# Performance work log

Hardware: AMD Instinct MI355X
Metric: run time of the kernel (lower is better)

Reference implementation:

```python
import jax, jax.numpy as jnp
import numpy as np

B, T, C, H = 4, 1024, 512, 4
D = C // H
N_LAYER, LAYER_ID = 12, 1


def setup_inputs() -> dict:
    key = jax.random.key(0)
    ks = jax.random.split(key, 10)
    w = lambda k, shape: 0.02 * jax.random.normal(k, shape, dtype=jnp.float32)

    r01 = LAYER_ID / (N_LAYER - 1)          # ratio_0_to_1
    r1a0 = 1.0 - LAYER_ID / N_LAYER          # ratio_1_to_almost0
    i = np.arange(C, dtype=np.float32)
    time_decay = (-5.0 + 8.0 * (i / (C - 1)) ** (0.7 + 1.3 * r01)).astype(np.float32)
    xv = i / C
    tm_q = (xv ** r1a0).astype(np.float32)[None, None, :]
    tm_k = (xv ** r1a0).astype(np.float32)[None, None, :]
    tm_v = ((xv ** r1a0) + 0.3 * r01).astype(np.float32)[None, None, :]
    tm_g = (xv ** (0.5 * r1a0)).astype(np.float32)[None, None, :]

    return dict(
        x=jax.random.normal(ks[0], (B, T, C), dtype=jnp.float32),
        ln1_g=jnp.ones((C,), jnp.float32), ln1_b=jnp.zeros((C,), jnp.float32),
        ln2_g=jnp.ones((C,), jnp.float32), ln2_b=jnp.zeros((C,), jnp.float32),
        time_decay=jnp.asarray(time_decay),
        tm_q=jnp.asarray(tm_q), tm_k=jnp.asarray(tm_k),
        tm_v=jnp.asarray(tm_v), tm_g=jnp.asarray(tm_g),
        Wq=w(ks[1], (C, C)), Wk=w(ks[2], (C, C)), Wv=w(ks[3], (C, C)),
        Wg=w(ks[4], (C, C)), Wo=w(ks[5], (C, C)),
        rms_scale=jnp.ones((C,), jnp.float32),
        W1=w(ks[6], (4 * C, C)), W2=w(ks[7], (C, 4 * C)),
    )


def layernorm(x, g, b, eps=1e-5):
    m = x.mean(-1, keepdims=True)
    v = ((x - m) ** 2).mean(-1, keepdims=True)
    return g * (x - m) / jnp.sqrt(v + eps) + b


def rmsnorm(x, scale, eps=1e-8):
    # matches: norm = ||x||_2 / sqrt(dim); out = scale * x / (norm + eps)
    norm = jnp.sqrt(jnp.sum(x * x, axis=-1, keepdims=True)) / (x.shape[-1] ** 0.5)
    return scale * (x / (norm + eps))


def lnssm_scan(q, k, v, lam):
    """Decayed linear-attention scan. q,k,v: [B,T,H,D]; lam: [H,D] (decay over k index).
    Returns S: [B,T,H,D] = q_t^T A_t, Zs: [B,T,H] = q_t . z_t."""
    qT, kT, vT = (jnp.moveaxis(a, 1, 0) for a in (q, k, v))  # [T,B,H,D]
    Bq = q.shape[0]
    A0 = jnp.zeros((Bq, q.shape[2], q.shape[3], q.shape[3]), q.dtype)
    z0 = jnp.zeros((Bq, q.shape[2], q.shape[3]), q.dtype)

    def step(carry, inp):
        A, z = carry
        qt, kt, vt = inp
        A = lam[None, :, :, None] * A + kt[..., None] * vt[..., None, :]  # [B,H,Dk,Dv]
        z = lam[None] * z + kt                                            # [B,H,Dk]
        St = jnp.einsum('bhi,bhij->bhj', qt, A)
        Zt = jnp.einsum('bhi,bhi->bh', qt, z)
        return (A, z), (St, Zt)

    _, (S, Zs) = jax.lax.scan(step, (A0, z0), (qT, kT, vT))
    return jnp.moveaxis(S, 0, 1), jnp.moveaxis(Zs, 0, 1)


def reference(x, ln1_g, ln1_b, ln2_g, ln2_b, time_decay, tm_q, tm_k, tm_v, tm_g,
              Wq, Wk, Wv, Wg, Wo, rms_scale, W1, W2):
    Bx, Tx, Cx = x.shape
    Hh, Dd = H, Cx // H

    # --- TimeMix on ln1(x) ---
    h = layernorm(x, ln1_g, ln1_b)
    xx = jnp.concatenate([jnp.zeros_like(h[:, :1]), h[:, :-1]], axis=1)  # time shift
    xq = h * tm_q + xx * (1 - tm_q)
    xk = h * tm_k + xx * (1 - tm_k)
    xv_ = h * tm_v + xx * (1 - tm_v)
    xg = h * tm_g + xx * (1 - tm_g)
    q = xq @ Wq.T
    k = xk @ Wk.T
    v = xv_ @ Wv.T
    g = jax.nn.sigmoid(xg @ Wg.T)
    q = jnp.exp(rmsnorm(q, rms_scale))
    k = jnp.exp(rmsnorm(k, rms_scale))

    lam = jnp.exp(-jnp.exp(time_decay)).reshape(Hh, Dd)
    qh = q.reshape(Bx, Tx, Hh, Dd)
    kh = k.reshape(Bx, Tx, Hh, Dd)
    vh = v.reshape(Bx, Tx, Hh, Dd)
    S, Zs = lnssm_scan(qh, kh, vh, lam)
    att = (S / Zs[..., None]).reshape(Bx, Tx, Cx)
    att = (g * att) @ Wo.T
    x = x + att

    # --- ChannelMix on ln2(x) ---
    h2 = layernorm(x, ln2_g, ln2_b)
    x = x + jax.nn.gelu(h2 @ W1.T, approximate=False) @ W2.T
    return x
```

## Files before the change

### kernel.cpp

```cpp
#include <hip/hip_runtime.h>
#include <math.h>

#define Bb 4
#define Tt 1024
#define Cc 512
#define Hh 4
#define Dd 128
#define Mrows (Bb*Tt)
#define NC 32
#define CL 32
#define AUGB_CB 18432

typedef unsigned short u16;
typedef __attribute__((ext_vector_type(8))) short bf16x8;
typedef __attribute__((ext_vector_type(4))) float f32x4;

__device__ __forceinline__ u16 f2bf(float f) {
  unsigned u = __float_as_uint(f);
  unsigned r = (u + 0x7fffu + ((u >> 16) & 1u)) >> 16;
  return (u16)r;
}
__device__ __forceinline__ float bf2f(u16 v) {
  return __uint_as_float((unsigned)v << 16);
}
__device__ __forceinline__ unsigned pack2(float a, float b) {
  return (unsigned)f2bf(a) | ((unsigned)f2bf(b) << 16);
}
__device__ __forceinline__ void unpack8(uint4 a, u16* o) {
  o[0]=(u16)a.x; o[1]=(u16)(a.x>>16);
  o[2]=(u16)a.y; o[3]=(u16)(a.y>>16);
  o[4]=(u16)a.z; o[5]=(u16)(a.z>>16);
  o[6]=(u16)a.w; o[7]=(u16)(a.w>>16);
}
__device__ __forceinline__ float rms_r(const float* __restrict__ ssqp, int zsel, int row) {
  const float* p = ssqp + (size_t)zsel*8*Mrows + row;
  float s2 = 0.f;
  #pragma unroll
  for (int u = 0; u < 8; ++u) s2 += p[(size_t)u*Mrows];
  float norm = sqrtf(s2) * 0.044194173824159216f;
  return 1.f / (norm + 1e-8f);
}

__global__ __launch_bounds__(256) void prep_kernel(const float* __restrict__ x,
    const float* __restrict__ g, const float* __restrict__ bta,
    const float* __restrict__ tmq, const float* __restrict__ tmk,
    const float* __restrict__ tmv, const float* __restrict__ tmg,
    u16* __restrict__ xqb, u16* __restrict__ xkb,
    u16* __restrict__ xvb, u16* __restrict__ xgb,
    const float* __restrict__ Wq, const float* __restrict__ Wk,
    const float* __restrict__ Wv, const float* __restrict__ Wg,
    const float* __restrict__ Wo, const float* __restrict__ W1,
    const float* __restrict__ W2, u16* __restrict__ wout)
{
  int tid = threadIdx.x;
  if (blockIdx.x >= 4096) {
    int blk = blockIdx.x - 4096;
    const float* src; u16* dst; int K, nshift;
    if (blk < 640) {
      int wsel = blk >> 7;
      src = wsel==0?Wq:wsel==1?Wk:wsel==2?Wv:wsel==3?Wg:Wo;
      dst = wout + (size_t)wsel*262144; K = 512; nshift = 9; blk &= 127;
    } else if (blk < 1152) {
      src = W1; dst = wout + (size_t)5*262144; K = 512; nshift = 11; blk -= 640;
    } else {
      src = W2; dst = wout + (size_t)5*262144 + 1048576; K = 2048; nshift = 9; blk -= 1152;
    }
    int i = blk*256 + tid;
    int n = i & ((1 << nshift) - 1), kg = i >> nshift;
    const float* p = src + (size_t)n * K + kg * 8;
    float4 a = *(const float4*)p, b = *(const float4*)(p + 4);
    uint4 o;
    o.x = pack2(a.x, a.y); o.y = pack2(a.z, a.w);
    o.z = pack2(b.x, b.y); o.w = pack2(b.z, b.w);
    *(uint4*)(dst + (size_t)i * 8) = o;
    return;
  }
  int m = blockIdx.x;
  const float* xr = x + (size_t)m * Cc;
  float v0 = xr[tid], v1 = xr[tid + 256];
  bool has = (m & (Tt-1)) != 0;
  float u0 = 0.f, u1 = 0.f;
  if (has) { u0 = xr[tid - Cc]; u1 = xr[(int)tid + 256 - Cc]; }
  float sa = v0 + v1, qa = v0*v0 + v1*v1;
  float sb = u0 + u1, qb2 = u0*u0 + u1*u1;
  #pragma unroll
  for (int off = 32; off > 0; off >>= 1) {
    sa += __shfl_down(sa, off, 64); qa += __shfl_down(qa, off, 64);
    sb += __shfl_down(sb, off, 64); qb2 += __shfl_down(qb2, off, 64);
  }
  __shared__ float r4[4][4];
  int w = tid >> 6;
  if ((tid & 63) == 0) { r4[w][0]=sa; r4[w][1]=qa; r4[w][2]=sb; r4[w][3]=qb2; }
  __syncthreads();
  float Sa = r4[0][0]+r4[1][0]+r4[2][0]+r4[3][0];
  float Qa = r4[0][1]+r4[1][1]+r4[2][1]+r4[3][1];
  float Sb = r4[0][2]+r4[1][2]+r4[2][2]+r4[3][2];
  float Qb = r4[0][3]+r4[1][3]+r4[2][3]+r4[3][3];
  float ma = Sa*(1.f/Cc), va = Qa*(1.f/Cc) - ma*ma, ia = rsqrtf(va + 1e-5f);
  float mb = Sb*(1.f/Cc), vb2 = Qb*(1.f/Cc) - mb*mb, ib = rsqrtf(vb2 + 1e-5f);
  #pragma unroll
  for (int half = 0; half < 2; ++half) {
    int c = tid + half*256;
    float v = half ? v1 : v0, u = half ? u1 : u0;
    float hv = g[c]*(v - ma)*ia + bta[c];
    float pv = has ? (g[c]*(u - mb)*ib + bta[c]) : 0.f;
    size_t off = ((size_t)(c >> 3) * Mrows + m) * 8 + (c & 7);
    float tq = tmq[c], tk = tmk[c], tv = tmv[c], tg = tmg[c];
    xqb[off] = f2bf(hv*tq + pv*(1.f-tq));
    xkb[off] = f2bf(hv*tk + pv*(1.f-tk));
    xvb[off] = f2bf(hv*tv + pv*(1.f-tv));
    xgb[off] = f2bf(hv*tg + pv*(1.f-tg));
  }
}

__global__ __launch_bounds__(256) void ln2b_kernel(const float* __restrict__ x,
    const float* __restrict__ p0,
    const float* __restrict__ g, const float* __restrict__ bta,
    float* __restrict__ x1, u16* __restrict__ out)
{
  int row = blockIdx.x, tid = threadIdx.x;
  size_t r0 = (size_t)row * Cc + tid, r1 = r0 + 256;
  float v0 = x[r0] + p0[r0];
  float v1 = x[r1] + p0[r1];
  x1[r0] = v0; x1[r1] = v1;
  float s = v0 + v1, s2 = v0*v0 + v1*v1;
  #pragma unroll
  for (int off = 32; off > 0; off >>= 1) {
    s  += __shfl_down(s,  off, 64);
    s2 += __shfl_down(s2, off, 64);
  }
  __shared__ float rs[4], rq[4];
  int w = tid >> 6;
  if ((tid & 63) == 0) { rs[w] = s; rq[w] = s2; }
  __syncthreads();
  float S  = rs[0]+rs[1]+rs[2]+rs[3];
  float S2 = rq[0]+rq[1]+rq[2]+rq[3];
  float mean = S * (1.0f/Cc);
  float var  = S2 * (1.0f/Cc) - mean*mean;
  float inv = rsqrtf(var + 1e-5f);
  int c0 = tid, c1 = tid + 256;
  float o0 = g[c0] * (v0-mean)*inv + bta[c0];
  float o1 = g[c1] * (v1-mean)*inv + bta[c1];
  out[((size_t)(c0 >> 3) * Mrows + row) * 8 + (c0 & 7)] = f2bf(o0);
  out[((size_t)(c1 >> 3) * Mrows + row) * 8 + (c1 & 7)] = f2bf(o1);
}

template<int MR, int NR, int KR>
__device__ __forceinline__ void gemm_core64(const u16* __restrict__ A,
    const u16* __restrict__ W, const float* __restrict__ res,
    float* __restrict__ outf, u16* __restrict__ outb, int act,
    int m0, int n0, u16* Asm, u16* Bsm, float* __restrict__ ssq)
{
  const int tid = threadIdx.x, w = tid >> 6, l = tid & 63;
  const int wr = w >> 1, wc = w & 1;
  f32x4 acc[2][2];
  #pragma unroll
  for (int i = 0; i < 2; ++i)
    #pragma unroll
    for (int j = 0; j < 2; ++j) acc[i][j] = (f32x4){0.f,0.f,0.f,0.f};
  const int kgl = l >> 4, rl = l & 15;
  const int q = w * 2;

  #define STAGE(KT, BUF) do {                                               \
    _Pragma("unroll")                                                       \
    for (int ii = 0; ii < 2; ++ii) {                                        \
      int qq = q + ii;                                                      \
      int isB = qq >> 2, kg = qq & 3;                                       \
      const u16* src = isB                                                  \
        ? W + ((size_t)((KT)*4 + kg) * NR + n0 + l) * 8                     \
        : A + ((size_t)((KT)*4 + kg) * MR + m0 + l) * 8;                    \
      u16* dst = (isB ? Bsm : Asm) + (BUF)*2048 + kg * 64 * 8;              \
      __builtin_amdgcn_global_load_lds(                                     \
          (const __attribute__((address_space(1))) void*)src,               \
          (__attribute__((address_space(3))) void*)dst, 16, 0, 0);          \
    }                                                                       \
  } while (0)

  constexpr int nk = KR >> 5;
  STAGE(0, 0); STAGE(1, 1);
  int cur = 0;
  for (int kt = 0; kt < nk; ++kt) {
    if (kt == nk - 1) asm volatile("s_waitcnt vmcnt(0)" ::: "memory");
    else              asm volatile("s_waitcnt vmcnt(2)" ::: "memory");
    __builtin_amdgcn_s_barrier();
    bf16x8 af[2], bfr[2];
    #pragma unroll
    for (int f = 0; f < 2; ++f)
      af[f] = *(const bf16x8*)&Asm[cur*2048 + (kgl*64 + wr*32 + f*16 + rl) * 8];
    #pragma unroll
    for (int f = 0; f < 2; ++f)
      bfr[f] = *(const bf16x8*)&Bsm[cur*2048 + (kgl*64 + wc*32 + f*16 + rl) * 8];
    if (kt + 2 < nk) {
      int nb = cur + 2; if (nb >= 3) nb -= 3;
      STAGE(kt + 2, nb);
    }
    __builtin_amdgcn_s_setprio(1);
    #pragma unroll
    for (int i = 0; i < 2; ++i)
      #pragma unroll
      for (int j = 0; j < 2; ++j)
        acc[i][j] = __builtin_amdgcn_mfma_f32_16x16x32_bf16(af[i], bfr[j], acc[i][j], 0, 0, 0);
    __builtin_amdgcn_s_setprio(0);
    if (++cur == 3) cur = 0;
  }
  #undef STAGE

  const int rbase = (l >> 4) * 4, cn = l & 15;
  #pragma unroll
  for (int i = 0; i < 2; ++i) {
    #pragma unroll
    for (int j = 0; j < 2; ++j) {
      #pragma unroll
      for (int r = 0; r < 4; ++r) {
        int m = m0 + wr*32 + i*16 + rbase + r;
        int n = n0 + wc*32 + j*16 + cn;
        float vv = acc[i][j][r];
        if (res) vv += res[(size_t)m * NR + n];
        if (act == 1) vv = 0.5f*vv*(1.f + erff(vv * 0.70710678118f));
        else if (act == 2) vv = 1.f/(1.f + expf(-vv));
        if (outb) outb[((size_t)(n >> 3) * MR + m) * 8 + (n & 7)] = f2bf(vv);
        else outf[(size_t)m * NR + n] = vv;
      }
    }
  }

  if (ssq) {
    __syncthreads();
    float* red2 = (float*)Asm;
    #pragma unroll
    for (int i = 0; i < 2; ++i) {
      #pragma unroll
      for (int r = 0; r < 4; ++r) {
        int row_local = wr*32 + i*16 + rbase + r;
        float sq = 0.f;
        #pragma unroll
        for (int j = 0; j < 2; ++j) { float t = acc[i][j][r]; sq += t*t; }
        red2[row_local*32 + wc*16 + cn] = sq;
      }
    }
    __syncthreads();
    if (tid < 64) {
      float ssum = 0.f;
      #pragma unroll
      for (int u2 = 0; u2 < 32; ++u2) ssum += red2[tid*32 + u2];
      ssq[m0 + tid] = ssum;
    }
  }
}

__global__ __launch_bounds__(256) void gemm_qkvg(const u16* __restrict__ xall,
    const u16* __restrict__ Wall, u16* __restrict__ outall, float* __restrict__ ssqp)
{
  __shared__ __align__(16) u16 Asm[3*2048];
  __shared__ __align__(16) u16 Bsm[3*2048];
  int z = blockIdx.z;
  const size_t E = (size_t)Mrows * Cc;
  float* ssq = (z < 2) ? ssqp + ((size_t)z*8 + blockIdx.x)*Mrows : nullptr;
  gemm_core64<Mrows,512,512>(xall + z*E, Wall + (size_t)z*262144, nullptr,
            nullptr, outall + z*E, z == 3 ? 2 : 0,
            blockIdx.y * 64, blockIdx.x * 64, Asm, Bsm, ssq);
}

__global__ __launch_bounds__(256) void gemm_wo(const u16* __restrict__ A,
    const u16* __restrict__ W, float* __restrict__ outf)
{
  __shared__ __align__(16) u16 Asm[3*2048];
  __shared__ __align__(16) u16 Bsm[3*2048];
  gemm_core64<Mrows,512,512>(A, W, nullptr, outf, nullptr, 0,
            blockIdx.y * 64, blockIdx.x * 64, Asm, Bsm, nullptr);
}

__global__ __launch_bounds__(256) void gemm_w1(const u16* __restrict__ A,
    const u16* __restrict__ W, u16* __restrict__ outb)
{
  __shared__ __align__(16) u16 Asm[3*2048];
  __shared__ __align__(16) u16 Bsm[3*2048];
  gemm_core64<Mrows,2048,512>(A, W, nullptr, nullptr, outb, 1,
            blockIdx.y * 64, blockIdx.x * 64, Asm, Bsm, nullptr);
}

__global__ __launch_bounds__(256) void gemm_w2(const u16* __restrict__ A,
    const u16* __restrict__ W, const float* __restrict__ res, float* __restrict__ outf)
{
  __shared__ __align__(16) u16 Asm[3*2048];
  __shared__ __align__(16) u16 Bsm[3*2048];
  gemm_core64<Mrows,512,2048>(A, W, res, outf, nullptr, 0,
            blockIdx.y * 64, blockIdx.x * 64, Asm, Bsm, nullptr);
}

__global__ __launch_bounds__(256) void chunk_state_kernel(const u16* __restrict__ kb,
    const u16* __restrict__ vb, const float* __restrict__ td,
    const float* __restrict__ rsc, const float* __restrict__ ssqp,
    u16* __restrict__ Augl)
{
  __shared__ float k_lds[CL][Dd];
  __shared__ float v_lds[CL][Dd];
  int blk = blockIdx.x; int c = blk & (NC-1); int bh = blk >> 5;
  int b = bh >> 2, h = bh & 3;
  int tid = threadIdx.x;
  #pragma unroll
  for (int r = 0; r < 4; ++r) {
    int idx4 = r*256 + tid;
    int s = idx4 >> 5; int i4 = (idx4 & 31) << 2;
    int m = b*Tt + c*CL + s;
    float rk = rms_r(ssqp, 1, m);
    int cidx = h*Dd + i4;
    size_t boff = ((size_t)(cidx >> 3) * Mrows + m) * 8 + (cidx & 7);
    uint2 kr = *(const uint2*)(kb + boff);
    uint2 vr = *(const uint2*)(vb + boff);
    k_lds[s][i4+0] = expf(rsc[h*Dd+i4+0] * bf2f((u16)kr.x) * rk);
    k_lds[s][i4+1] = expf(rsc[h*Dd+i4+1] * bf2f((u16)(kr.x>>16)) * rk);
    k_lds[s][i4+2] = expf(rsc[h*Dd+i4+2] * bf2f((u16)kr.y) * rk);
    k_lds[s][i4+3] = expf(rsc[h*Dd+i4+3] * bf2f((u16)(kr.y>>16)) * rk);
    v_lds[s][i4+0] = bf2f((u16)vr.x);
    v_lds[s][i4+1] = bf2f((u16)(vr.x>>16));
    v_lds[s][i4+2] = bf2f((u16)vr.y);
    v_lds[s][i4+3] = bf2f((u16)(vr.y>>16));
  }
  __syncthreads();
  int iq = tid >> 3; int i0 = iq << 2;
  int jg = tid & 7;  int j0 = jg << 4;
  float lam4[4], powv[4], zacc[4];
  #pragma unroll
  for (int ci=0; ci<4; ++ci) {
    lam4[ci] = expf(-expf(td[h*Dd + i0 + ci]));
    powv[ci] = 1.f; zacc[ci] = 0.f;
  }
  float acc[4][16];
  #pragma unroll
  for (int ci=0; ci<4; ++ci)
    #pragma unroll
    for (int jj=0; jj<16; ++jj) acc[ci][jj] = 0.f;

  for (int s = CL-1; s >= 0; --s) {
    float4 k4 = *(const float4*)&k_lds[s][i0];
    float kw0 = powv[0]*k4.x, kw1 = powv[1]*k4.y, kw2 = powv[2]*k4.z, kw3 = powv[3]*k4.w;
    zacc[0]+=kw0; zacc[1]+=kw1; zacc[2]+=kw2; zacc[3]+=kw3;
    #pragma unroll
    for (int q4 = 0; q4 < 4; ++q4) {
      float4 v4 = *(const float4*)&v_lds[s][j0 + q4*4];
      float vv[4] = {v4.x, v4.y, v4.z, v4.w};
      #pragma unroll
      for (int u=0; u<4; ++u) {
        acc[0][q4*4+u] += kw0*vv[u];
        acc[1][q4*4+u] += kw1*vv[u];
        acc[2][q4*4+u] += kw2*vv[u];
        acc[3][q4*4+u] += kw3*vv[u];
      }
    }
    powv[0]*=lam4[0]; powv[1]*=lam4[1]; powv[2]*=lam4[2]; powv[3]*=lam4[3];
  }
  u16* aug = Augl + ((size_t)c*16 + bh)*AUGB_CB;
  const int ig = i0 >> 3, isub = i0 & 7;
  #pragma unroll
  for (int jj=0; jj<16; ++jj) {
    int j = j0 + jj;
    uint2 pk;
    pk.x = pack2(acc[0][jj], acc[1][jj]);
    pk.y = pack2(acc[2][jj], acc[3][jj]);
    *(uint2*)&aug[(size_t)ig*1152 + (size_t)j*8 + isub] = pk;
  }
  if (jg == 0) {
    uint2 pk;
    pk.x = pack2(zacc[0], zacc[1]);
    pk.y = pack2(zacc[2], zacc[3]);
    *(uint2*)&aug[(size_t)ig*1152 + 128*8 + isub] = pk;
  }
}

__global__ __launch_bounds__(256) void combine_kernel(const u16* __restrict__ Augl,
    const float* __restrict__ td, u16* __restrict__ Augb)
{
  int idx = blockIdx.x*256 + threadIdx.x;
  if (idx >= 129*128) return;
  int bh = blockIdx.y; int h = bh & 3;
  int j = idx >> 7, i = idx & 127;
  size_t aoff = (size_t)(i >> 3) * 1152 + (size_t)j * 8 + (i & 7);
  float lamL = expf(-expf(td[h*Dd + i]) * (float)CL);
  const u16* pl = Augl + (size_t)bh*AUGB_CB + aoff;
  u16* pi = Augb + (size_t)bh*AUGB_CB + aoff;
  float prev = 0.f;
  const size_t cstr = (size_t)16*AUGB_CB;
  for (int c = 0; c < NC; ++c) {
    float val = bf2f(pl[c*cstr]);
    pi[c*cstr] = f2bf(prev);
    prev = lamL*prev + val;
  }
}

__global__ __launch_bounds__(256, 2) void scan_mfma_kernel(
    const u16* __restrict__ qb, const u16* __restrict__ kb,
    const u16* __restrict__ vb, const float* __restrict__ td,
    const float* __restrict__ rsc, const float* __restrict__ ssqp,
    const u16* __restrict__ Augb, const u16* __restrict__ gb,
    u16* __restrict__ out)
{
  __shared__ float k_lds[32*192];
  __shared__ u16  qfrag[32*128];
  __shared__ u16  vfrag[4*1152];
  __shared__ float P32[32*33];
  __shared__ u16  pfrag[32*32];
  __shared__ float lam_lds[128];
  __shared__ float zbuf[32];

  const int tid = threadIdx.x;
  const int blk = blockIdx.x; const int c = blk & 31, bh = blk >> 5;
  const int b = bh >> 2, h = bh & 3;
  const int w = tid >> 6, l = tid & 63;
  const int t = (w << 3) + (l >> 3);
  const int is = l & 7;

  if (tid < 128) lam_lds[tid] = expf(-expf(td[h*Dd + tid]));

  const int grow = b*Tt + c*CL + t;
  const float rq = rms_r(ssqp, 0, grow);
  const float rk = rms_r(ssqp, 1, grow);
  const int g0 = (h*Dd + is*16) >> 3;
  const size_t bbase = ((size_t)g0*Mrows + grow)*8;

  float qv[16];
  {
    uint4 qA = *(const uint4*)(qb + bbase);
    uint4 qB = *(const uint4*)(qb + bbase + (size_t)Mrows*8);
    u16 qraw[16];
    unpack8(qA, qraw); unpack8(qB, qraw + 8);
    #pragma unroll
    for (int e = 0; e < 16; ++e)
      qv[e] = expf(rsc[h*Dd + is*16 + e] * bf2f(qraw[e]) * rq);
    float lt = (float)(t + 1);
    u16 qt[16];
    #pragma unroll
    for (int e = 0; e < 16; ++e) {
      float el2 = -expf(td[h*Dd + is*16 + e]) * 1.4426950408889634f;
      qt[e] = f2bf(qv[e] * exp2f(el2 * lt));
    }
    #pragma unroll
    for (int hf = 0; hf < 2; ++hf) {
      int k8 = is*2 + hf;
      uint4 pk;
      pk.x = (unsigned)qt[hf*8+0] | ((unsigned)qt[hf*8+1]<<16);
      pk.y = (unsigned)qt[hf*8+2] | ((unsigned)qt[hf*8+3]<<16);
      pk.z = (unsigned)qt[hf*8+4] | ((unsigned)qt[hf*8+5]<<16);
      pk.w = (unsigned)qt[hf*8+6] | ((unsigned)qt[hf*8+7]<<16);
      *(uint4*)&qfrag[t*128 + ((k8 ^ (t&7))<<3)] = pk;
    }
  }
  {
    uint4 kA = *(const uint4*)(kb + bbase);
    uint4 kB = *(const uint4*)(kb + bbase + (size_t)Mrows*8);
    u16 kraw[16];
    unpack8(kA, kraw); unpack8(kB, kraw + 8);
    #pragma unroll
    for (int e = 0; e < 16; ++e)
      k_lds[t*192 + is*24 + e] = expf(rsc[h*Dd + is*16 + e] * bf2f(kraw[e]) * rk);
  }
  {
    uint4 vA = *(const uint4*)(vb + bbase);
    uint4 vB = *(const uint4*)(vb + bbase + (size_t)Mrows*8);
    u16 vraw[16];
    unpack8(vA, vraw); unpack8(vB, vraw + 8);
    #pragma unroll
    for (int e = 0; e < 16; ++e)
      vfrag[(t>>3)*1152 + (is*16 + e)*8 + (t&7)] = vraw[e];
  }
  if (tid < 32) vfrag[(tid>>3)*1152 + 128*8 + (tid&7)] = 0x3F80;
  if (tid < 240) {
    #pragma unroll
    for (int u = 0; u < 2; ++u) {
      int e = tid*2 + u;
      int ig = e / 120, rem = e % 120;
      vfrag[ig*1152 + (129 + rem/8)*8 + (rem&7)] = 0;
    }
  }
  __syncthreads();

  {
    float lamr[16], wrun[16];
    #pragma unroll
    for (int e4 = 0; e4 < 4; ++e4) {
      float4 l4 = *(const float4*)&lam_lds[is*16 + e4*4];
      lamr[e4*4+0]=l4.x; lamr[e4*4+1]=l4.y; lamr[e4*4+2]=l4.z; lamr[e4*4+3]=l4.w;
    }
    #pragma unroll
    for (int e = 0; e < 16; ++e) wrun[e] = 1.f;
    const int smax = (w << 3) + 7;
    for (int s = smax; s >= 0; --s) {
      float dot = 0.f;
      #pragma unroll
      for (int c4 = 0; c4 < 4; ++c4) {
        float4 k4 = *(const float4*)&k_lds[s*192 + is*24 + c4*4];
        dot = fmaf(qv[c4*4+0], k4.x*wrun[c4*4+0], dot);
        dot = fmaf(qv[c4*4+1], k4.y*wrun[c4*4+1], dot);
        dot = fmaf(qv[c4*4+2], k4.z*wrun[c4*4+2], dot);
        dot = fmaf(qv[c4*4+3], k4.w*wrun[c4*4+3], dot);
      }
      dot += __shfl_xor(dot, 1);
      dot += __shfl_xor(dot, 2);
      dot += __shfl_xor(dot, 4);
      bool act = (s <= t);
      if (act && is == 0) P32[t*33 + s] = dot;
      if (act) {
        #pragma unroll
        for (int e = 0; e < 16; ++e) wrun[e] *= lamr[e];
      }
    }
  }
  __syncthreads();
  {
    int tt = tid >> 3, s0 = (tid & 7) * 4;
    #pragma unroll
    for (int ss = 0; ss < 4; ++ss) {
      int s = s0 + ss;
      float val = (s <= tt) ? P32[tt*33 + s] : 0.f;
      pfrag[tt*32 + (((s>>3) ^ (tt&3))<<3) + (s&7)] = f2bf(val);
    }
  }
  __syncthreads();

  const int tau = w >> 1;
  const int jt0 = (w & 1) ? 5 : 0;
  const int njt = (w & 1) ? 4 : 5;
  const int rl = l & 15, kg = l >> 4;
  const int trow = tau*16 + rl;
  const u16* augb_base = Augb + ((size_t)c*16 + bh)*AUGB_CB;

  bf16x8 aq[4];
  #pragma unroll
  for (int kk = 0; kk < 4; ++kk)
    aq[kk] = *(const bf16x8*)&qfrag[trow*128 + ((((kk<<2)+kg) ^ (trow&7))<<3)];
  bf16x8 ap = *(const bf16x8*)&pfrag[trow*32 + ((kg ^ (trow&3))<<3)];

  f32x4 acc[5];
  #pragma unroll
  for (int u = 0; u < 5; ++u) acc[u] = (f32x4){0.f,0.f,0.f,0.f};

  #pragma unroll
  for (int u = 0; u < 5; ++u) {
    if (u < njt) {
      int jt = jt0 + u;
      #pragma unroll
      for (int kk = 0; kk < 4; ++kk) {
        bf16x8 bfr = *(const bf16x8*)&augb_base[(size_t)(((kk<<2)+kg)*1152 + (jt*16 + rl)*8)];
        acc[u] = __builtin_amdgcn_mfma_f32_16x16x32_bf16(aq[kk], bfr, acc[u], 0, 0, 0);
      }
      bf16x8 bv = *(const bf16x8*)&vfrag[kg*1152 + (jt*16 + rl)*8];
      acc[u] = __builtin_amdgcn_mfma_f32_16x16x32_bf16(ap, bv, acc[u], 0, 0, 0);
    }
  }
  if ((w & 1) && rl == 0) {
    #pragma unroll
    for (int r = 0; r < 4; ++r) zbuf[tau*16 + kg*4 + r] = acc[3][r];
  }
  __syncthreads();

  const int nout = (w & 1) ? 3 : 5;
  #pragma unroll
  for (int u = 0; u < 5; ++u) {
    if (u < nout) {
      int jt = jt0 + u;
      int cc = h*Dd + jt*16 + rl;
      #pragma unroll
      for (int r = 0; r < 4; ++r) {
        int tr = tau*16 + kg*4 + r;
        int m = b*Tt + c*CL + tr;
        float zv = zbuf[tr];
        float gv = bf2f(gb[((size_t)(cc >> 3) * Mrows + m) * 8 + (cc & 7)]);
        out[((size_t)(cc >> 3) * Mrows + m) * 8 + (cc & 7)] = f2bf(gv * acc[u][r] / zv);
      }
    }
  }
}

extern "C" void kernel_launch(void* const* d_in, const int* in_sizes, int n_in,
                              void* d_out, int out_size, void* d_ws, size_t ws_size,
                              hipStream_t stream) {
  const float* x    = (const float*)d_in[0];
  const float* ln1g = (const float*)d_in[1];
  const float* ln1b = (const float*)d_in[2];
  const float* ln2g = (const float*)d_in[3];
  const float* ln2b = (const float*)d_in[4];
  const float* td   = (const float*)d_in[5];
  const float* tmq  = (const float*)d_in[6];
  const float* tmk  = (const float*)d_in[7];
  const float* tmv  = (const float*)d_in[8];
  const float* tmg  = (const float*)d_in[9];
  const float* Wq   = (const float*)d_in[10];
  const float* Wk   = (const float*)d_in[11];
  const float* Wv   = (const float*)d_in[12];
  const float* Wg   = (const float*)d_in[13];
  const float* Wo   = (const float*)d_in[14];
  const float* rsc  = (const float*)d_in[15];
  const float* W1   = (const float*)d_in[16];
  const float* W2   = (const float*)d_in[17];
  float* ws = (float*)d_ws;
  const size_t E = (size_t)Mrows*Cc;
  float* x1 = ws;
  float* s2 = ws + E;
  u16* ub  = (u16*)(ws + 2*E);
  u16* xqb = ub;
  u16* xkb = xqb + E;
  u16* xvb = xkb + E;
  u16* xgb = xvb + E;
  u16* qb  = ub + 4*E;
  u16* kb  = qb + E;
  u16* vb  = kb + E;
  u16* gb  = vb + E;
  u16* Wqb = ub + 8*E;
  u16* Wob = Wqb + 4*262144;
  u16* W1b = Wqb + 5*262144;
  u16* W2b = W1b + 1048576;
  u16* Augl = W2b + 1048576;
  u16* Augb = Augl + (size_t)NC*16*AUGB_CB;
  float* ssqp = (float*)(Augb + (size_t)NC*16*AUGB_CB);
  u16* midb  = Augl;
  u16* gattb = xqb;
  u16* h2b   = xkb;

  prep_kernel<<<5760,256,0,stream>>>(x, ln1g, ln1b, tmq,tmk,tmv,tmg,
                                     xqb,xkb,xvb,xgb,
                                     Wq, Wk, Wv, Wg, Wo, W1, W2, Wqb);
  gemm_qkvg<<<dim3(8,64,4),256,0,stream>>>(xqb, Wqb, qb, ssqp);
  chunk_state_kernel<<<16*NC,256,0,stream>>>(kb, vb, td, rsc, ssqp, Augl);
  combine_kernel<<<dim3(65,16),256,0,stream>>>(Augl, td, Augb);
  scan_mfma_kernel<<<16*NC,256,0,stream>>>(qb, kb, vb, td, rsc, ssqp, Augb, gb, gattb);
  gemm_wo<<<dim3(8,64),256,0,stream>>>(gattb, Wob, s2);
  ln2b_kernel<<<Mrows,256,0,stream>>>(x, s2, ln2g, ln2b, x1, h2b);
  gemm_w1<<<dim3(32,64),256,0,stream>>>(h2b, W1b, midb);
  gemm_w2<<<dim3(8,64),256,0,stream>>>(midb, W2b, x1, (float*)d_out);
}
```

Before: 169.5 us.

## Load GEMM MFMA fragments directly from global memory into registers, dropping LDS staging

```diff
diff --git a/kernel.cpp b/kernel.cpp
--- a/kernel.cpp
+++ b/kernel.cpp
@@ -146,64 +146,57 @@
 }
 
 template<int MR, int NR, int KR>
-__device__ __forceinline__ void gemm_core64(const u16* __restrict__ A,
+__device__ __forceinline__ void gemm_reg64(const u16* __restrict__ A,
     const u16* __restrict__ W, const float* __restrict__ res,
     float* __restrict__ outf, u16* __restrict__ outb, int act,
-    int m0, int n0, u16* Asm, u16* Bsm, float* __restrict__ ssq)
+    int m0, int n0, float* __restrict__ ssq, float* __restrict__ red2)
 {
   const int tid = threadIdx.x, w = tid >> 6, l = tid & 63;
   const int wr = w >> 1, wc = w & 1;
+  const int kgl = l >> 4, rl = l & 15;
   f32x4 acc[2][2];
   #pragma unroll
   for (int i = 0; i < 2; ++i)
     #pragma unroll
     for (int j = 0; j < 2; ++j) acc[i][j] = (f32x4){0.f,0.f,0.f,0.f};
-  const int kgl = l >> 4, rl = l & 15;
-  const int q = w * 2;
-
-  #define STAGE(KT, BUF) do {                                               \
-    _Pragma("unroll")                                                       \
-    for (int ii = 0; ii < 2; ++ii) {                                        \
-      int qq = q + ii;                                                      \
-      int isB = qq >> 2, kg = qq & 3;                                       \
-      const u16* src = isB                                                  \
-        ? W + ((size_t)((KT)*4 + kg) * NR + n0 + l) * 8                     \
-        : A + ((size_t)((KT)*4 + kg) * MR + m0 + l) * 8;                    \
-      u16* dst = (isB ? Bsm : Asm) + (BUF)*2048 + kg * 64 * 8;              \
-      __builtin_amdgcn_global_load_lds(                                     \
-          (const __attribute__((address_space(1))) void*)src,               \
-          (__attribute__((address_space(3))) void*)dst, 16, 0, 0);          \
-    }                                                                       \
+
+  const u16* ap = A + ((size_t)kgl * MR + m0 + wr*32 + rl) * 8;
+  const u16* bp = W + ((size_t)kgl * NR + n0 + wc*32 + rl) * 8;
+  const size_t astep = (size_t)4 * MR * 8;
+  const size_t bstep = (size_t)4 * NR * 8;
+
+  #define LDFRAGS(KT, AV, BV) do {                                   \
+    const u16* ap_ = ap + (size_t)(KT) * astep;                      \
+    AV[0] = *(const bf16x8*)(ap_);                                   \
+    AV[1] = *(const bf16x8*)(ap_ + 16*8);                            \
+    const u16* bp_ = bp + (size_t)(KT) * bstep;                      \
+    BV[0] = *(const bf16x8*)(bp_);                                   \
+    BV[1] = *(const bf16x8*)(bp_ + 16*8);                            \
   } while (0)
 
   constexpr int nk = KR >> 5;
-  STAGE(0, 0); STAGE(1, 1);
-  int cur = 0;
-  for (int kt = 0; kt < nk; ++kt) {
-    if (kt == nk - 1) asm volatile("s_waitcnt vmcnt(0)" ::: "memory");
-    else              asm volatile("s_waitcnt vmcnt(2)" ::: "memory");
-    __builtin_amdgcn_s_barrier();
-    bf16x8 af[2], bfr[2];
-    #pragma unroll
-    for (int f = 0; f < 2; ++f)
-      af[f] = *(const bf16x8*)&Asm[cur*2048 + (kgl*64 + wr*32 + f*16 + rl) * 8];
-    #pragma unroll
-    for (int f = 0; f < 2; ++f)
-      bfr[f] = *(const bf16x8*)&Bsm[cur*2048 + (kgl*64 + wc*32 + f*16 + rl) * 8];
-    if (kt + 2 < nk) {
-      int nb = cur + 2; if (nb >= 3) nb -= 3;
-      STAGE(kt + 2, nb);
-    }
+  bf16x8 aA[2], bA[2], aB[2], bB[2];
+  LDFRAGS(0, aA, bA);
+  LDFRAGS(1, aB, bB);
+  for (int kt = 0; kt < nk; kt += 2) {
     __builtin_amdgcn_s_setprio(1);
     #pragma unroll
     for (int i = 0; i < 2; ++i)
       #pragma unroll
       for (int j = 0; j < 2; ++j)
-        acc[i][j] = __builtin_amdgcn_mfma_f32_16x16x32_bf16(af[i], bfr[j], acc[i][j], 0, 0, 0);
+        acc[i][j] = __builtin_amdgcn_mfma_f32_16x16x32_bf16(aA[i], bA[j], acc[i][j], 0, 0, 0);
     __builtin_amdgcn_s_setprio(0);
-    if (++cur == 3) cur = 0;
-  }
-  #undef STAGE
+    if (kt + 2 < nk) LDFRAGS(kt + 2, aA, bA);
+    __builtin_amdgcn_s_setprio(1);
+    #pragma unroll
+    for (int i = 0; i < 2; ++i)
+      #pragma unroll
+      for (int j = 0; j < 2; ++j)
+        acc[i][j] = __builtin_amdgcn_mfma_f32_16x16x32_bf16(aB[i], bB[j], acc[i][j], 0, 0, 0);
+    __builtin_amdgcn_s_setprio(0);
+    if (kt + 3 < nk) LDFRAGS(kt + 3, aB, bB);
+  }
+  #undef LDFRAGS
 
   const int rbase = (l >> 4) * 4, cn = l & 15;
   #pragma unroll
@@ -226,7 +219,6 @@
 
   if (ssq) {
     __syncthreads();
-    float* red2 = (float*)Asm;
     #pragma unroll
     for (int i = 0; i < 2; ++i) {
       #pragma unroll
@@ -251,41 +243,34 @@
 __global__ __launch_bounds__(256) void gemm_qkvg(const u16* __restrict__ xall,
     const u16* __restrict__ Wall, u16* __restrict__ outall, float* __restrict__ ssqp)
 {
-  __shared__ __align__(16) u16 Asm[3*2048];
-  __shared__ __align__(16) u16 Bsm[3*2048];
+  __shared__ float red2[64*32];
   int z = blockIdx.z;
   const size_t E = (size_t)Mrows * Cc;
   float* ssq = (z < 2) ? ssqp + ((size_t)z*8 + blockIdx.x)*Mrows : nullptr;
-  gemm_core64<Mrows,512,512>(xall + z*E, Wall + (size_t)z*262144, nullptr,
+  gemm_reg64<Mrows,512,512>(xall + z*E, Wall + (size_t)z*262144, nullptr,
             nullptr, outall + z*E, z == 3 ? 2 : 0,
-            blockIdx.y * 64, blockIdx.x * 64, Asm, Bsm, ssq);
+            blockIdx.y * 64, blockIdx.x * 64, ssq, red2);
 }
 
 __global__ __launch_bounds__(256) void gemm_wo(const u16* __restrict__ A,
     const u16* __restrict__ W, float* __restrict__ outf)
 {
-  __shared__ __align__(16) u16 Asm[3*2048];
-  __shared__ __align__(16) u16 Bsm[3*2048];
-  gemm_core64<Mrows,512,512>(A, W, nullptr, outf, nullptr, 0,
-            blockIdx.y * 64, blockIdx.x * 64, Asm, Bsm, nullptr);
+  gemm_reg64<Mrows,512,512>(A, W, nullptr, outf, nullptr, 0,
+            blockIdx.y * 64, blockIdx.x * 64, nullptr, nullptr);
 }
 
 __global__ __launch_bounds__(256) void gemm_w1(const u16* __restrict__ A,
     const u16* __restrict__ W, u16* __restrict__ outb)
 {
-  __shared__ __align__(16) u16 Asm[3*2048];
-  __shared__ __align__(16) u16 Bsm[3*2048];
-  gemm_core64<Mrows,2048,512>(A, W, nullptr, nullptr, outb, 1,
-            blockIdx.y * 64, blockIdx.x * 64, Asm, Bsm, nullptr);
+  gemm_reg64<Mrows,2048,512>(A, W, nullptr, nullptr, outb, 1,
+            blockIdx.y * 64, blockIdx.x * 64, nullptr, nullptr);
 }
 
 __global__ __launch_bounds__(256) void gemm_w2(const u16* __restrict__ A,
     const u16* __restrict__ W, const float* __restrict__ res, float* __restrict__ outf)
 {
-  __shared__ __align__(16) u16 Asm[3*2048];
-  __shared__ __align__(16) u16 Bsm[3*2048];
-  gemm_core64<Mrows,512,2048>(A, W, res, outf, nullptr, 0,
-            blockIdx.y * 64, blockIdx.x * 64, Asm, Bsm, nullptr);
+  gemm_reg64<Mrows,512,2048>(A, W, res, outf, nullptr, 0,
+            blockIdx.y * 64, blockIdx.x * 64, nullptr, nullptr);
 }
 
 __global__ __launch_bounds__(256) void chunk_state_kernel(const u16* __restrict__ kb,
```

Result: slower. 175.0 us (+3.2%).

## Enlarge GEMM tiles to 128x128 and split-K the Wo and W2 GEMMs

Applied to the files above, without the earlier changes.

```diff
diff --git a/kernel.cpp b/kernel.cpp
--- a/kernel.cpp
+++ b/kernel.cpp
@@ -33,10 +33,8 @@
   o[6]=(u16)a.w; o[7]=(u16)(a.w>>16);
 }
 __device__ __forceinline__ float rms_r(const float* __restrict__ ssqp, int zsel, int row) {
-  const float* p = ssqp + (size_t)zsel*8*Mrows + row;
-  float s2 = 0.f;
-  #pragma unroll
-  for (int u = 0; u < 8; ++u) s2 += p[(size_t)u*Mrows];
+  const float* p = ssqp + (size_t)zsel*4*Mrows + row;
+  float s2 = p[0] + p[Mrows] + p[2*Mrows] + p[3*Mrows];
   float norm = sqrtf(s2) * 0.044194173824159216f;
   return 1.f / (norm + 1e-8f);
 }
@@ -114,14 +112,14 @@
 }
 
 __global__ __launch_bounds__(256) void ln2b_kernel(const float* __restrict__ x,
-    const float* __restrict__ p0,
+    const float* __restrict__ p0, const float* __restrict__ p1,
     const float* __restrict__ g, const float* __restrict__ bta,
     float* __restrict__ x1, u16* __restrict__ out)
 {
   int row = blockIdx.x, tid = threadIdx.x;
   size_t r0 = (size_t)row * Cc + tid, r1 = r0 + 256;
-  float v0 = x[r0] + p0[r0];
-  float v1 = x[r1] + p0[r1];
+  float v0 = x[r0] + p0[r0] + p1[r0];
+  float v1 = x[r1] + p0[r1] + p1[r1];
   x1[r0] = v0; x1[r1] = v1;
   float s = v0 + v1, s2 = v0*v0 + v1*v1;
   #pragma unroll
@@ -146,30 +144,30 @@
 }
 
 template<int MR, int NR, int KR>
-__device__ __forceinline__ void gemm_core64(const u16* __restrict__ A,
+__device__ __forceinline__ void gemm_core(const u16* __restrict__ A,
     const u16* __restrict__ W, const float* __restrict__ res,
     float* __restrict__ outf, u16* __restrict__ outb, int act,
     int m0, int n0, u16* Asm, u16* Bsm, float* __restrict__ ssq)
 {
   const int tid = threadIdx.x, w = tid >> 6, l = tid & 63;
   const int wr = w >> 1, wc = w & 1;
-  f32x4 acc[2][2];
-  #pragma unroll
-  for (int i = 0; i < 2; ++i)
-    #pragma unroll
-    for (int j = 0; j < 2; ++j) acc[i][j] = (f32x4){0.f,0.f,0.f,0.f};
+  f32x4 acc[4][4];
+  #pragma unroll
+  for (int i = 0; i < 4; ++i)
+    #pragma unroll
+    for (int j = 0; j < 4; ++j) acc[i][j] = (f32x4){0.f,0.f,0.f,0.f};
   const int kgl = l >> 4, rl = l & 15;
-  const int q = w * 2;
+  const int q = w * 4;
 
   #define STAGE(KT, BUF) do {                                               \
     _Pragma("unroll")                                                       \
-    for (int ii = 0; ii < 2; ++ii) {                                        \
+    for (int ii = 0; ii < 4; ++ii) {                                        \
       int qq = q + ii;                                                      \
-      int isB = qq >> 2, kg = qq & 3;                                       \
+      int isB = qq >> 3, idx = qq & 7, kg = idx >> 1, hf = idx & 1;         \
       const u16* src = isB                                                  \
-        ? W + ((size_t)((KT)*4 + kg) * NR + n0 + l) * 8                     \
-        : A + ((size_t)((KT)*4 + kg) * MR + m0 + l) * 8;                    \
-      u16* dst = (isB ? Bsm : Asm) + (BUF)*2048 + kg * 64 * 8;              \
+        ? W + ((size_t)((KT)*4 + kg) * NR + n0 + hf*64 + l) * 8             \
+        : A + ((size_t)((KT)*4 + kg) * MR + m0 + hf*64 + l) * 8;            \
+      u16* dst = (isB ? Bsm : Asm) + (BUF)*4096 + (kg * 128 + hf * 64) * 8; \
       __builtin_amdgcn_global_load_lds(                                     \
           (const __attribute__((address_space(1))) void*)src,               \
           (__attribute__((address_space(3))) void*)dst, 16, 0, 0);          \
@@ -181,24 +179,24 @@
   int cur = 0;
   for (int kt = 0; kt < nk; ++kt) {
     if (kt == nk - 1) asm volatile("s_waitcnt vmcnt(0)" ::: "memory");
-    else              asm volatile("s_waitcnt vmcnt(2)" ::: "memory");
+    else              asm volatile("s_waitcnt vmcnt(4)" ::: "memory");
     __builtin_amdgcn_s_barrier();
-    bf16x8 af[2], bfr[2];
-    #pragma unroll
-    for (int f = 0; f < 2; ++f)
-      af[f] = *(const bf16x8*)&Asm[cur*2048 + (kgl*64 + wr*32 + f*16 + rl) * 8];
-    #pragma unroll
-    for (int f = 0; f < 2; ++f)
-      bfr[f] = *(const bf16x8*)&Bsm[cur*2048 + (kgl*64 + wc*32 + f*16 + rl) * 8];
+    bf16x8 af[4], bfr[4];
+    #pragma unroll
+    for (int f = 0; f < 4; ++f)
+      af[f] = *(const bf16x8*)&Asm[cur*4096 + (kgl*128 + wr*64 + f*16 + rl) * 8];
+    #pragma unroll
+    for (int f = 0; f < 4; ++f)
+      bfr[f] = *(const bf16x8*)&Bsm[cur*4096 + (kgl*128 + wc*64 + f*16 + rl) * 8];
     if (kt + 2 < nk) {
       int nb = cur + 2; if (nb >= 3) nb -= 3;
       STAGE(kt + 2, nb);
     }
     __builtin_amdgcn_s_setprio(1);
     #pragma unroll
-    for (int i = 0; i < 2; ++i)
-      #pragma unroll
-      for (int j = 0; j < 2; ++j)
+    for (int i = 0; i < 4; ++i)
+      #pragma unroll
+      for (int j = 0; j < 4; ++j)
         acc[i][j] = __builtin_amdgcn_mfma_f32_16x16x32_bf16(af[i], bfr[j], acc[i][j], 0, 0, 0);
     __builtin_amdgcn_s_setprio(0);
     if (++cur == 3) cur = 0;
@@ -207,13 +205,13 @@
 
   const int rbase = (l >> 4) * 4, cn = l & 15;
   #pragma unroll
-  for (int i = 0; i < 2; ++i) {
-    #pragma unroll
-    for (int j = 0; j < 2; ++j) {
+  for (int i = 0; i < 4; ++i) {
+    #pragma unroll
+    for (int j = 0; j < 4; ++j) {
       #pragma unroll
       for (int r = 0; r < 4; ++r) {
-        int m = m0 + wr*32 + i*16 + rbase + r;
-        int n = n0 + wc*32 + j*16 + cn;
+        int m = m0 + wr*64 + i*16 + rbase + r;
+        int n = n0 + wc*64 + j*16 + cn;
         float vv = acc[i][j][r];
         if (res) vv += res[(size_t)m * NR + n];
         if (act == 1) vv = 0.5f*vv*(1.f + erff(vv * 0.70710678118f));
@@ -228,18 +226,18 @@
     __syncthreads();
     float* red2 = (float*)Asm;
     #pragma unroll
-    for (int i = 0; i < 2; ++i) {
+    for (int i = 0; i < 4; ++i) {
       #pragma unroll
       for (int r = 0; r < 4; ++r) {
-        int row_local = wr*32 + i*16 + rbase + r;
+        int row_local = wr*64 + i*16 + rbase + r;
         float sq = 0.f;
         #pragma unroll
-        for (int j = 0; j < 2; ++j) { float t = acc[i][j][r]; sq += t*t; }
+        for (int j = 0; j < 4; ++j) { float t = acc[i][j][r]; sq += t*t; }
         red2[row_local*32 + wc*16 + cn] = sq;
       }
     }
     __syncthreads();
-    if (tid < 64) {
+    if (tid < 128) {
       float ssum = 0.f;
       #pragma unroll
       for (int u2 = 0; u2 < 32; ++u2) ssum += red2[tid*32 + u2];
@@ -251,41 +249,61 @@
 __global__ __launch_bounds__(256) void gemm_qkvg(const u16* __restrict__ xall,
     const u16* __restrict__ Wall, u16* __restrict__ outall, float* __restrict__ ssqp)
 {
-  __shared__ __align__(16) u16 Asm[3*2048];
-  __shared__ __align__(16) u16 Bsm[3*2048];
+  __shared__ __align__(16) u16 Asm[3*4096];
+  __shared__ __align__(16) u16 Bsm[3*4096];
   int z = blockIdx.z;
   const size_t E = (size_t)Mrows * Cc;
-  float* ssq = (z < 2) ? ssqp + ((size_t)z*8 + blockIdx.x)*Mrows : nullptr;
-  gemm_core64<Mrows,512,512>(xall + z*E, Wall + (size_t)z*262144, nullptr,
+  float* ssq = (z < 2) ? ssqp + ((size_t)z*4 + blockIdx.x)*Mrows : nullptr;
+  gemm_core<Mrows,512,512>(xall + z*E, Wall + (size_t)z*262144, nullptr,
             nullptr, outall + z*E, z == 3 ? 2 : 0,
-            blockIdx.y * 64, blockIdx.x * 64, Asm, Bsm, ssq);
+            blockIdx.y * 128, blockIdx.x * 128, Asm, Bsm, ssq);
 }
 
 __global__ __launch_bounds__(256) void gemm_wo(const u16* __restrict__ A,
-    const u16* __restrict__ W, float* __restrict__ outf)
-{
-  __shared__ __align__(16) u16 Asm[3*2048];
-  __shared__ __align__(16) u16 Bsm[3*2048];
-  gemm_core64<Mrows,512,512>(A, W, nullptr, outf, nullptr, 0,
-            blockIdx.y * 64, blockIdx.x * 64, Asm, Bsm, nullptr);
+    const u16* __restrict__ W, float* __restrict__ pbuf)
+{
+  __shared__ __align__(16) u16 Asm[3*4096];
+  __shared__ __align__(16) u16 Bsm[3*4096];
+  int z = blockIdx.z;
+  const size_t E = (size_t)Mrows * Cc;
+  gemm_core<Mrows,512,256>(A + (size_t)z*32*Mrows*8, W + (size_t)z*32*512*8, nullptr,
+            pbuf + z*E, nullptr, 0, blockIdx.y * 128, blockIdx.x * 128, Asm, Bsm, nullptr);
 }
 
 __global__ __launch_bounds__(256) void gemm_w1(const u16* __restrict__ A,
     const u16* __restrict__ W, u16* __restrict__ outb)
 {
-  __shared__ __align__(16) u16 Asm[3*2048];
-  __shared__ __align__(16) u16 Bsm[3*2048];
-  gemm_core64<Mrows,2048,512>(A, W, nullptr, nullptr, outb, 1,
-            blockIdx.y * 64, blockIdx.x * 64, Asm, Bsm, nullptr);
+  __shared__ __align__(16) u16 Asm[3*4096];
+  __shared__ __align__(16) u16 Bsm[3*4096];
+  gemm_core<Mrows,2048,512>(A, W, nullptr, nullptr, outb, 1,
+            blockIdx.y * 128, blockIdx.x * 128, Asm, Bsm, nullptr);
 }
 
 __global__ __launch_bounds__(256) void gemm_w2(const u16* __restrict__ A,
-    const u16* __restrict__ W, const float* __restrict__ res, float* __restrict__ outf)
-{
-  __shared__ __align__(16) u16 Asm[3*2048];
-  __shared__ __align__(16) u16 Bsm[3*2048];
-  gemm_core64<Mrows,512,2048>(A, W, res, outf, nullptr, 0,
-            blockIdx.y * 64, blockIdx.x * 64, Asm, Bsm, nullptr);
+    const u16* __restrict__ W, float* __restrict__ pbuf)
+{
+  __shared__ __align__(16) u16 Asm[3*4096];
+  __shared__ __align__(16) u16 Bsm[3*4096];
+  int z = blockIdx.z;
+  const size_t E = (size_t)Mrows * Cc;
+  gemm_core<Mrows,512,1024>(A + (size_t)z*128*Mrows*8, W + (size_t)z*128*512*8, nullptr,
+            pbuf + z*E, nullptr, 0, blockIdx.y * 128, blockIdx.x * 128, Asm, Bsm, nullptr);
+}
+
+__global__ __launch_bounds__(256) void reduce2_kernel(const float* __restrict__ x1,
+    const float* __restrict__ p, float* __restrict__ out)
+{
+  const size_t E = (size_t)Mrows * Cc;
+  size_t f = ((size_t)blockIdx.x * 256 + threadIdx.x) * 4;
+  float4 a = *(const float4*)(x1 + f);
+  float4 q0 = *(const float4*)(p + f);
+  float4 q1 = *(const float4*)(p + E + f);
+  float4 o;
+  o.x = a.x + q0.x + q1.x;
+  o.y = a.y + q0.y + q1.y;
+  o.z = a.z + q0.z + q1.z;
+  o.w = a.w + q0.w + q1.w;
+  *(float4*)(out + f) = o;
 }
 
 __global__ __launch_bounds__(256) void chunk_state_kernel(const u16* __restrict__ kb,
@@ -381,6 +399,7 @@
   u16* pi = Augb + (size_t)bh*AUGB_CB + aoff;
   float prev = 0.f;
   const size_t cstr = (size_t)16*AUGB_CB;
+  #pragma unroll
   for (int c = 0; c < NC; ++c) {
     float val = bf2f(pl[c*cstr]);
     pi[c*cstr] = f2bf(prev);
@@ -595,8 +614,8 @@
   float* ws = (float*)d_ws;
   const size_t E = (size_t)Mrows*Cc;
   float* x1 = ws;
-  float* s2 = ws + E;
-  u16* ub  = (u16*)(ws + 2*E);
+  float* pb = ws + E;
+  u16* ub  = (u16*)(ws + 3*E);
   u16* xqb = ub;
   u16* xkb = xqb + E;
   u16* xvb = xkb + E;
@@ -619,12 +638,13 @@
   prep_kernel<<<5760,256,0,stream>>>(x, ln1g, ln1b, tmq,tmk,tmv,tmg,
                                      xqb,xkb,xvb,xgb,
                                      Wq, Wk, Wv, Wg, Wo, W1, W2, Wqb);
-  gemm_qkvg<<<dim3(8,64,4),256,0,stream>>>(xqb, Wqb, qb, ssqp);
+  gemm_qkvg<<<dim3(4,32,4),256,0,stream>>>(xqb, Wqb, qb, ssqp);
   chunk_state_kernel<<<16*NC,256,0,stream>>>(kb, vb, td, rsc, ssqp, Augl);
   combine_kernel<<<dim3(65,16),256,0,stream>>>(Augl, td, Augb);
   scan_mfma_kernel<<<16*NC,256,0,stream>>>(qb, kb, vb, td, rsc, ssqp, Augb, gb, gattb);
-  gemm_wo<<<dim3(8,64),256,0,stream>>>(gattb, Wob, s2);
-  ln2b_kernel<<<Mrows,256,0,stream>>>(x, s2, ln2g, ln2b, x1, h2b);
-  gemm_w1<<<dim3(32,64),256,0,stream>>>(h2b, W1b, midb);
-  gemm_w2<<<dim3(8,64),256,0,stream>>>(midb, W2b, x1, (float*)d_out);
-}
+  gemm_wo<<<dim3(4,32,2),256,0,stream>>>(gattb, Wob, pb);
+  ln2b_kernel<<<Mrows,256,0,stream>>>(x, pb, pb + E, ln2g, ln2b, x1, h2b);
+  gemm_w1<<<dim3(16,32),256,0,stream>>>(h2b, W1b, midb);
+  gemm_w2<<<dim3(4,32,2),256,0,stream>>>(midb, W2b, pb);
+  reduce2_kernel<<<2048,256,0,stream>>>(x1, pb, (float*)d_out);
+}
```

After: 169.2 us. About the same (-0.2%).
